# Performance work log

Hardware: AMD Instinct MI355X
Metric: run time of the kernel (lower is better)

## Reference

```python
import jax, jax.numpy as jnp
import numpy as np

N_NODES = 100000
N_EDGES = 1600000

def gcn_conv(x, src, dst, W, b, n):
    # symmetric GCN normalization with self-loops already included in src/dst
    deg = jax.ops.segment_sum(jnp.ones_like(src, dtype=x.dtype), dst, num_segments=n)
    dinv = jnp.where(deg > 0, jax.lax.rsqrt(deg), 0.0)
    norm = dinv[src] * dinv[dst]            # [E]
    h = x @ W                                # [n, out]
    msg = h[src] * norm[:, None]             # gather + scale, [E, out]
    out = jax.ops.segment_sum(msg, dst, num_segments=n)  # scatter-add
    return out + b

def setup_inputs() -> dict:
    key = jax.random.key(0)
    k1, k2, k3, k4 = jax.random.split(key, 4)
    x = jax.random.normal(k1, (N_NODES, 768), dtype=jnp.float32)
    edge_index = jax.random.randint(k2, (2, N_EDGES), 0, N_NODES, dtype=jnp.int64)
    W1 = jax.random.normal(k3, (768, 64), dtype=jnp.float32) * (1.0 / np.sqrt(768))
    b1 = jnp.zeros((64,), dtype=jnp.float32)
    W2 = jax.random.normal(k4, (64, 32), dtype=jnp.float32) * (1.0 / np.sqrt(64))
    b2 = jnp.zeros((32,), dtype=jnp.float32)
    return {"x": x, "edge_index": edge_index, "W1": W1, "b1": b1, "W2": W2, "b2": b2}

def reference(x, edge_index, W1, b1, W2, b2):
    n = x.shape[0]
    loop = jnp.arange(n, dtype=edge_index.dtype)
    src = jnp.concatenate([edge_index[0], loop])
    dst = jnp.concatenate([edge_index[1], loop])
    h = jax.nn.relu(gcn_conv(x, src, dst, W1, b1, n))
    # F.dropout with training=False -> identity (eval mode)
    out = gcn_conv(h, src, dst, W2, b2, n)
    return out
```

## Files before the change

kernel.cpp:

```cpp
#include <hip/hip_runtime.h>


constexpr int C1 = 64;
constexpr int C2 = 32;
constexpr int K1 = 768;
constexpr int SCAN_BS = 256;
constexpr int SCAN_ELEMS = 2048;

typedef __attribute__((ext_vector_type(8))) short short8;
typedef __attribute__((ext_vector_type(4))) float floatx4;

__global__ void detect_k(const int* __restrict__ ei32, int* flag, int n_words) {
    __shared__ int any_nz;
    if (threadIdx.x == 0) any_nz = 0;
    __syncthreads();
    int w = 2 * threadIdx.x + 1;
    if (w < n_words && ei32[w] != 0) atomicOr(&any_nz, 1);
    __syncthreads();
    if (threadIdx.x == 0) *flag = (any_nz == 0) ? 1 : 0;
}

__device__ __forceinline__ int load_idx(const void* ei, size_t pos, int m64) {
    if (m64) return (int)((const long long*)ei)[pos];
    return ((const int*)ei)[pos];
}

__global__ void zero_k(int* p, int n) {
    int i = blockIdx.x * 256 + threadIdx.x;
    if (i < n) p[i] = 0;
}

__global__ void cnt_k(const void* __restrict__ ei, const int* __restrict__ flag,
                      int* cnt, int E) {
    int e = blockIdx.x * 256 + threadIdx.x;
    if (e >= E) return;
    int m64 = *flag;
    int d = load_idx(ei, (size_t)E + e, m64);
    atomicAdd(&cnt[d], 1);
}

__global__ void dinv_k(const int* __restrict__ cnt, float* dinv, int n) {
    int i = blockIdx.x * 256 + threadIdx.x;
    if (i < n) dinv[i] = rsqrtf(1.0f + (float)cnt[i]);
}

__global__ void scan1_k(const int* __restrict__ cnt, int* partials, int n) {
    __shared__ int s[SCAN_BS];
    int base = blockIdx.x * SCAN_ELEMS;
    int t = threadIdx.x;
    int sum = 0;
    #pragma unroll
    for (int i = 0; i < 8; ++i) {
        int idx = base + t * 8 + i;
        if (idx < n) sum += cnt[idx];
    }
    s[t] = sum;
    __syncthreads();
    for (int off = 128; off > 0; off >>= 1) {
        if (t < off) s[t] += s[t + off];
        __syncthreads();
    }
    if (t == 0) partials[blockIdx.x] = s[0];
}

__global__ void scan2_k(int* partials, int* total_out, int nb) {
    __shared__ int s[256];
    int t = threadIdx.x;
    int v = (t < nb) ? partials[t] : 0;
    s[t] = v;
    __syncthreads();
    for (int off = 1; off < 256; off <<= 1) {
        int add = (t >= off) ? s[t - off] : 0;
        __syncthreads();
        s[t] += add;
        __syncthreads();
    }
    if (t < nb) partials[t] = s[t] - v;
    if (t == 0) *total_out = s[255];
}

__global__ void scan3_k(const int* __restrict__ cnt, const int* __restrict__ partials,
                        int* offsets, int* cursor, int n) {
    __shared__ int s[SCAN_BS];
    int base = blockIdx.x * SCAN_ELEMS;
    int t = threadIdx.x;
    int local[8];
    int sum = 0;
    #pragma unroll
    for (int i = 0; i < 8; ++i) {
        int idx = base + t * 8 + i;
        int v = (idx < n) ? cnt[idx] : 0;
        local[i] = sum;
        sum += v;
    }
    int mine = sum;
    s[t] = sum;
    __syncthreads();
    for (int off = 1; off < 256; off <<= 1) {
        int add = (t >= off) ? s[t - off] : 0;
        __syncthreads();
        s[t] += add;
        __syncthreads();
    }
    int texcl = s[t] - mine;
    int boff = partials[blockIdx.x];
    #pragma unroll
    for (int i = 0; i < 8; ++i) {
        int idx = base + t * 8 + i;
        if (idx < n) {
            int o = boff + texcl + local[i];
            offsets[idx] = o;
            cursor[idx] = o;
        }
    }
}

__global__ void fill_k(const void* __restrict__ ei, const int* __restrict__ flag,
                       int* cursor, int* adj, int E) {
    int e = blockIdx.x * 256 + threadIdx.x;
    if (e >= E) return;
    int m64 = *flag;
    int s = load_idx(ei, e, m64);
    int d = load_idx(ei, (size_t)E + e, m64);
    int pos = atomicAdd(&cursor[d], 1);
    adj[pos] = s;
}

__device__ __forceinline__ void bf16_split(float f, short& hi, short& lo) {
    unsigned int u = __float_as_uint(f);
    unsigned int r = u + (0x7FFFu + ((u >> 16) & 1u));
    hi = (short)(r >> 16);
    float rem = f - __uint_as_float(r & 0xFFFF0000u);
    lo = (short)(__float_as_uint(rem) >> 16);
}

__global__ void packW1_k(const float* __restrict__ W1, unsigned short* __restrict__ Bp) {
    int gid = blockIdx.x * 256 + threadIdx.x;
    if (gid >= 24 * 4 * 2 * 64) return;
    int l    = gid & 63;
    int frag = gid >> 6;
    int p = frag & 1;
    int t = (frag >> 1) & 3;
    int s = frag >> 3;
    int c = t * 16 + (l & 15);
    int kbase = s * 32 + (l >> 4) * 8;
    short8 v;
    #pragma unroll
    for (int j = 0; j < 8; ++j) {
        short hi, lo;
        bf16_split(W1[(size_t)(kbase + j) * C1 + c], hi, lo);
        v[j] = p ? lo : hi;
    }
    *(short8*)(Bp + (size_t)gid * 8) = v;
}

__global__ __launch_bounds__(256) void gemm1_k(const float* __restrict__ x,
                                               const unsigned short* __restrict__ Bp,
                                               const float* __restrict__ dinv,
                                               float* __restrict__ g1, int n) {
    constexpr int MT = 128;
    __shared__ alignas(16) float As[2][MT * 32];
    __shared__ alignas(16) unsigned short Bs[2][4096];
    const int tid = threadIdx.x;
    const int w = tid >> 6;
    const int l = tid & 63;
    const int block_row = blockIdx.x * MT;

    floatx4 zero = {0.f, 0.f, 0.f, 0.f};
    floatx4 acc[2][4];
    #pragma unroll
    for (int r = 0; r < 2; ++r)
        #pragma unroll
        for (int t = 0; t < 4; ++t) acc[r][t] = zero;

    const int srow = l >> 3;
    const int skb  = (l & 7) ^ srow;

    auto stage = [&](int s, int b) {
        const int k0 = s * 32;
        #pragma unroll
        for (int gi = 0; gi < 4; ++gi) {
            int g = w * 4 + gi;
            int row = block_row + g * 8 + srow;
            if (row > n - 1) row = n - 1;
            const float* src = x + (size_t)row * K1 + k0 + skb * 4;
            __builtin_amdgcn_global_load_lds(
                (const __attribute__((address_space(1))) void*)src,
                (__attribute__((address_space(3))) void*)&As[b][g * 256], 16, 0, 0);
        }
        #pragma unroll
        for (int gi = 0; gi < 2; ++gi) {
            int j = w * 2 + gi;
            const unsigned short* src = Bp + (size_t)s * 4096 + j * 512 + l * 8;
            __builtin_amdgcn_global_load_lds(
                (const __attribute__((address_space(1))) void*)src,
                (__attribute__((address_space(3))) void*)&Bs[b][j * 512], 16, 0, 0);
        }
    };

    stage(0, 0);

    for (int t = 0; t < 24; ++t) {
        int nxt = (t + 1 < 24) ? t + 1 : 23;
        stage(nxt, (t + 1) & 1);

        asm volatile("s_waitcnt vmcnt(6)" ::: "memory");
        __builtin_amdgcn_s_barrier();

        const float* A = As[t & 1];
        const unsigned short* B = Bs[t & 1];

        short8 bh[4], bl[4];
        #pragma unroll
        for (int tt = 0; tt < 4; ++tt) {
            bh[tt] = *(const short8*)(B + (tt * 2 + 0) * 512 + l * 8);
            bl[tt] = *(const short8*)(B + (tt * 2 + 1) * 512 + l * 8);
        }

        #pragma unroll
        for (int r = 0; r < 2; ++r) {
            int row_local = w * 32 + r * 16 + (l & 15);
            int swz = l & 7;
            int kb0 = ((l >> 4) * 2) ^ swz;
            floatx4 f0 = *(const floatx4*)&A[row_local * 32 + kb0 * 4];
            floatx4 f1 = *(const floatx4*)&A[row_local * 32 + (kb0 ^ 1) * 4];
            short8 ah, al;
            float fv[8] = {f0[0], f0[1], f0[2], f0[3], f1[0], f1[1], f1[2], f1[3]};
            #pragma unroll
            for (int j = 0; j < 8; ++j) {
                short h16, l16;
                bf16_split(fv[j], h16, l16);
                ah[j] = h16;
                al[j] = l16;
            }
            #pragma unroll
            for (int tt = 0; tt < 4; ++tt) {
                acc[r][tt] = __builtin_amdgcn_mfma_f32_16x16x32_bf16(ah, bh[tt], acc[r][tt], 0, 0, 0);
                acc[r][tt] = __builtin_amdgcn_mfma_f32_16x16x32_bf16(al, bh[tt], acc[r][tt], 0, 0, 0);
                acc[r][tt] = __builtin_amdgcn_mfma_f32_16x16x32_bf16(ah, bl[tt], acc[r][tt], 0, 0, 0);
            }
        }

        __builtin_amdgcn_s_barrier();
    }

    #pragma unroll
    for (int r = 0; r < 2; ++r) {
        #pragma unroll
        for (int i = 0; i < 4; ++i) {
            int row = block_row + w * 32 + r * 16 + (l >> 4) * 4 + i;
            if (row < n) {
                float dv = dinv[row];
                #pragma unroll
                for (int t = 0; t < 4; ++t) {
                    g1[(size_t)row * C1 + t * 16 + (l & 15)] = acc[r][t][i] * dv;
                }
            }
        }
    }
}

__global__ __launch_bounds__(256) void gather1_k(const int* __restrict__ offsets,
                                                 const int* __restrict__ adj,
                                                 const float* __restrict__ dinv,
                                                 const float* __restrict__ g1,
                                                 const float* __restrict__ b1,
                                                 const float* __restrict__ W2,
                                                 float* __restrict__ g2, int n) {
    __shared__ float sW[C1 * C2];
    __shared__ float srow[4][C1];
    const int tid = threadIdx.x;
    for (int i = tid; i < C1 * C2; i += 256) sW[i] = W2[i];

    const int wid = tid >> 6;
    const int c = tid & 63;
    const int v = blockIdx.x * 4 + wid;

    float r = 0.f;
    float dv = 0.f;
    if (v < n) {
        dv = dinv[v];
        int start = offsets[v], end = offsets[v + 1];
        float acc = g1[(size_t)v * C1 + c];
        int j = start;
        for (; j + 4 <= end; j += 4) {
            int s0 = adj[j], s1 = adj[j + 1], s2 = adj[j + 2], s3 = adj[j + 3];
            float a0 = g1[(size_t)s0 * C1 + c];
            float a1 = g1[(size_t)s1 * C1 + c];
            float a2 = g1[(size_t)s2 * C1 + c];
            float a3 = g1[(size_t)s3 * C1 + c];
            acc += (a0 + a1) + (a2 + a3);
        }
        for (; j < end; ++j) acc += g1[(size_t)adj[j] * C1 + c];
        r = fmaxf(b1[c] + dv * acc, 0.f);
    }
    srow[wid][c] = r;
    __syncthreads();

    if (v < n && c < C2) {
        float acc = 0.f;
        #pragma unroll
        for (int k = 0; k < C1; ++k) acc += srow[wid][k] * sW[k * C2 + c];
        g2[(size_t)v * C2 + c] = dv * acc;
    }
}

__global__ __launch_bounds__(256) void gather2_k(const int* __restrict__ offsets,
                                                 const int* __restrict__ adj,
                                                 const float* __restrict__ dinv,
                                                 const float* __restrict__ g2,
                                                 const float* __restrict__ b2,
                                                 float* __restrict__ out, int n) {
    int v = blockIdx.x * 8 + (threadIdx.x >> 5);
    int c = threadIdx.x & 31;
    if (v >= n) return;
    int start = offsets[v], end = offsets[v + 1];
    float acc = g2[(size_t)v * C2 + c];
    int j = start;
    for (; j + 4 <= end; j += 4) {
        int s0 = adj[j], s1 = adj[j + 1], s2 = adj[j + 2], s3 = adj[j + 3];
        float a0 = g2[(size_t)s0 * C2 + c];
        float a1 = g2[(size_t)s1 * C2 + c];
        float a2 = g2[(size_t)s2 * C2 + c];
        float a3 = g2[(size_t)s3 * C2 + c];
        acc += (a0 + a1) + (a2 + a3);
    }
    for (; j < end; ++j) acc += g2[(size_t)adj[j] * C2 + c];
    out[(size_t)v * C2 + c] = b2[c] + dinv[v] * acc;
}

extern "C" void kernel_launch(void* const* d_in, const int* in_sizes, int n_in,
                              void* d_out, int out_size, void* d_ws, size_t ws_size,
                              hipStream_t stream) {
    const float* x  = (const float*)d_in[0];
    const void*  ei = d_in[1];
    const float* W1 = (const float*)d_in[2];
    const float* b1 = (const float*)d_in[3];
    const float* W2 = (const float*)d_in[4];
    const float* b2 = (const float*)d_in[5];
    float* out = (float*)d_out;

    const int n = in_sizes[0] / K1;
    const int E = in_sizes[1] / 2;

    float* ws      = (float*)d_ws;
    int*   flag    = (int*)ws;
    float* dinv    = ws + 16;
    float* g1      = dinv + n;
    float* g2      = g1 + (size_t)n * C1;
    int*   cnt     = (int*)(g2 + (size_t)n * C2);
    int*   offsets = cnt + n;
    int*   cursor  = offsets + n + 1;
    int*   partials= cursor + n;
    int*   adj     = partials + 256;
    uintptr_t bp_a = ((uintptr_t)(adj + E) + 15) & ~(uintptr_t)15;
    unsigned short* Bp = (unsigned short*)bp_a;

    const int nb_scan = (n + SCAN_ELEMS - 1) / SCAN_ELEMS;

    detect_k<<<1, 256, 0, stream>>>((const int*)ei, flag, in_sizes[1]);
    zero_k<<<(n + 255) / 256, 256, 0, stream>>>(cnt, n);
    cnt_k<<<(E + 255) / 256, 256, 0, stream>>>(ei, flag, cnt, E);
    dinv_k<<<(n + 255) / 256, 256, 0, stream>>>(cnt, dinv, n);

    packW1_k<<<48, 256, 0, stream>>>(W1, Bp);
    gemm1_k<<<(n + 127) / 128, 256, 0, stream>>>(x, Bp, dinv, g1, n);

    scan1_k<<<nb_scan, SCAN_BS, 0, stream>>>(cnt, partials, n);
    scan2_k<<<1, 256, 0, stream>>>(partials, offsets + n, nb_scan);
    scan3_k<<<nb_scan, SCAN_BS, 0, stream>>>(cnt, partials, offsets, cursor, n);
    fill_k<<<(E + 255) / 256, 256, 0, stream>>>(ei, flag, cursor, adj, E);

    gather1_k<<<(n + 3) / 4, 256, 0, stream>>>(offsets, adj, dinv, g1, b1, W2, g2, n);
    gather2_k<<<(n + 7) / 8, 256, 0, stream>>>(offsets, adj, dinv, g2, b2, out, n);
}
```

Before: 816.7 us.

## Load GEMM1 operands directly into registers, dropping LDS staging and barriers

Rewrites the first GEMM so each lane loads its A-fragment rows of x straight from global memory into registers, prefetching the next K step, and reads packed W1 fragments directly from global instead of staging both through LDS with barriers. It also reorders the split-bf16 MFMAs (small terms first) and sets a launch-bounds occupancy hint of 3. This removes LDS traffic and block-wide synchronisation. In exchange, W1 fragments are re-read from global/L2 by every wave, and the x loads are less coalesced, since each lane fetches 32 contiguous bytes from a different row.

```diff
diff --git a/kernel.cpp b/kernel.cpp
--- a/kernel.cpp
+++ b/kernel.cpp
@@ -132,6 +132,18 @@
     hi = (short)(r >> 16);
     float rem = f - __uint_as_float(r & 0xFFFF0000u);
     lo = (short)(__float_as_uint(rem) >> 16);
+}
+
+__device__ __forceinline__ void split8(const float4& a, const float4& b,
+                                       short8& h, short8& v) {
+    float f[8] = {a.x, a.y, a.z, a.w, b.x, b.y, b.z, b.w};
+    #pragma unroll
+    for (int j = 0; j < 8; ++j) {
+        short hh, ll;
+        bf16_split(f[j], hh, ll);
+        h[j] = hh;
+        v[j] = ll;
+    }
 }
 
 __global__ void packW1_k(const float* __restrict__ W1, unsigned short* __restrict__ Bp) {
@@ -154,17 +166,23 @@
     *(short8*)(Bp + (size_t)gid * 8) = v;
 }
 
-__global__ __launch_bounds__(256) void gemm1_k(const float* __restrict__ x,
-                                               const unsigned short* __restrict__ Bp,
-                                               const float* __restrict__ dinv,
-                                               float* __restrict__ g1, int n) {
-    constexpr int MT = 128;
-    __shared__ alignas(16) float As[2][MT * 32];
-    __shared__ alignas(16) unsigned short Bs[2][4096];
+__global__ __launch_bounds__(256, 3) void gemm1_k(const float* __restrict__ x,
+                                                  const unsigned short* __restrict__ Bp,
+                                                  const float* __restrict__ dinv,
+                                                  float* __restrict__ g1, int n) {
     const int tid = threadIdx.x;
     const int w = tid >> 6;
     const int l = tid & 63;
-    const int block_row = blockIdx.x * MT;
+    const int block_row = blockIdx.x * 128;
+    const int wrow = block_row + w * 32;
+
+    int row0 = wrow + (l & 15);        if (row0 > n - 1) row0 = n - 1;
+    int row1 = wrow + 16 + (l & 15);   if (row1 > n - 1) row1 = n - 1;
+    const int kl = (l >> 4) * 8;
+
+    const float* __restrict__ pa0 = x + (size_t)row0 * K1 + kl;
+    const float* __restrict__ pa1 = x + (size_t)row1 * K1 + kl;
+    const unsigned short* __restrict__ pb = Bp + l * 8;
 
     floatx4 zero = {0.f, 0.f, 0.f, 0.f};
     floatx4 acc[2][4];
@@ -173,75 +191,41 @@
         #pragma unroll
         for (int t = 0; t < 4; ++t) acc[r][t] = zero;
 
-    const int srow = l >> 3;
-    const int skb  = (l & 7) ^ srow;
-
-    auto stage = [&](int s, int b) {
-        const int k0 = s * 32;
-        #pragma unroll
-        for (int gi = 0; gi < 4; ++gi) {
-            int g = w * 4 + gi;
-            int row = block_row + g * 8 + srow;
-            if (row > n - 1) row = n - 1;
-            const float* src = x + (size_t)row * K1 + k0 + skb * 4;
-            __builtin_amdgcn_global_load_lds(
-                (const __attribute__((address_space(1))) void*)src,
-                (__attribute__((address_space(3))) void*)&As[b][g * 256], 16, 0, 0);
-        }
-        #pragma unroll
-        for (int gi = 0; gi < 2; ++gi) {
-            int j = w * 2 + gi;
-            const unsigned short* src = Bp + (size_t)s * 4096 + j * 512 + l * 8;
-            __builtin_amdgcn_global_load_lds(
-                (const __attribute__((address_space(1))) void*)src,
-                (__attribute__((address_space(3))) void*)&Bs[b][j * 512], 16, 0, 0);
-        }
-    };
-
-    stage(0, 0);
+    float4 a0a = *(const float4*)(pa0 + 0);
+    float4 a0b = *(const float4*)(pa0 + 4);
+    float4 a1a = *(const float4*)(pa1 + 0);
+    float4 a1b = *(const float4*)(pa1 + 4);
 
     for (int t = 0; t < 24; ++t) {
-        int nxt = (t + 1 < 24) ? t + 1 : 23;
-        stage(nxt, (t + 1) & 1);
-
-        asm volatile("s_waitcnt vmcnt(6)" ::: "memory");
-        __builtin_amdgcn_s_barrier();
-
-        const float* A = As[t & 1];
-        const unsigned short* B = Bs[t & 1];
-
+        const int tn = (t + 1 < 24) ? (t + 1) * 32 : 0;
+        float4 n0a = *(const float4*)(pa0 + tn);
+        float4 n0b = *(const float4*)(pa0 + tn + 4);
+        float4 n1a = *(const float4*)(pa1 + tn);
+        float4 n1b = *(const float4*)(pa1 + tn + 4);
+
+        const unsigned short* bt = pb + t * 4096;
         short8 bh[4], bl[4];
         #pragma unroll
         for (int tt = 0; tt < 4; ++tt) {
-            bh[tt] = *(const short8*)(B + (tt * 2 + 0) * 512 + l * 8);
-            bl[tt] = *(const short8*)(B + (tt * 2 + 1) * 512 + l * 8);
-        }
-
-        #pragma unroll
-        for (int r = 0; r < 2; ++r) {
-            int row_local = w * 32 + r * 16 + (l & 15);
-            int swz = l & 7;
-            int kb0 = ((l >> 4) * 2) ^ swz;
-            floatx4 f0 = *(const floatx4*)&A[row_local * 32 + kb0 * 4];
-            floatx4 f1 = *(const floatx4*)&A[row_local * 32 + (kb0 ^ 1) * 4];
-            short8 ah, al;
-            float fv[8] = {f0[0], f0[1], f0[2], f0[3], f1[0], f1[1], f1[2], f1[3]};
-            #pragma unroll
-            for (int j = 0; j < 8; ++j) {
-                short h16, l16;
-                bf16_split(fv[j], h16, l16);
-                ah[j] = h16;
-                al[j] = l16;
-            }
-            #pragma unroll
-            for (int tt = 0; tt < 4; ++tt) {
-                acc[r][tt] = __builtin_amdgcn_mfma_f32_16x16x32_bf16(ah, bh[tt], acc[r][tt], 0, 0, 0);
-                acc[r][tt] = __builtin_amdgcn_mfma_f32_16x16x32_bf16(al, bh[tt], acc[r][tt], 0, 0, 0);
-                acc[r][tt] = __builtin_amdgcn_mfma_f32_16x16x32_bf16(ah, bl[tt], acc[r][tt], 0, 0, 0);
-            }
-        }
-
-        __builtin_amdgcn_s_barrier();
+            bh[tt] = *(const short8*)(bt + (tt * 2 + 0) * 512);
+            bl[tt] = *(const short8*)(bt + (tt * 2 + 1) * 512);
+        }
+
+        short8 ah0, al0, ah1, al1;
+        split8(a0a, a0b, ah0, al0);
+        split8(a1a, a1b, ah1, al1);
+
+        #pragma unroll
+        for (int tt = 0; tt < 4; ++tt) {
+            acc[0][tt] = __builtin_amdgcn_mfma_f32_16x16x32_bf16(ah0, bl[tt], acc[0][tt], 0, 0, 0);
+            acc[0][tt] = __builtin_amdgcn_mfma_f32_16x16x32_bf16(al0, bh[tt], acc[0][tt], 0, 0, 0);
+            acc[0][tt] = __builtin_amdgcn_mfma_f32_16x16x32_bf16(ah0, bh[tt], acc[0][tt], 0, 0, 0);
+            acc[1][tt] = __builtin_amdgcn_mfma_f32_16x16x32_bf16(ah1, bl[tt], acc[1][tt], 0, 0, 0);
+            acc[1][tt] = __builtin_amdgcn_mfma_f32_16x16x32_bf16(al1, bh[tt], acc[1][tt], 0, 0, 0);
+            acc[1][tt] = __builtin_amdgcn_mfma_f32_16x16x32_bf16(ah1, bh[tt], acc[1][tt], 0, 0, 0);
+        }
+
+        a0a = n0a; a0b = n0b; a1a = n1a; a1b = n1b;
     }
 
     #pragma unroll
```

After: 818.8 us. Within noise of the previous version (+0.3%).
